# Kernel optimization log

Measured on AMD Instinct MI355X. Metric: run time of the kernel, lower is better.

## Reference

```python
import jax, jax.numpy as jnp
import numpy as np

# Llama-7B FFN up-proj quantized with HQQ 4-bit, group_size=64, axis=0
OUT, IN, GS = 11008, 4096, 64
G = OUT * IN // GS  # 704512 groups


def setup_inputs() -> dict:
    key = jax.random.key(0)
    k1, k2, k3, k4, k5 = jax.random.split(key, 5)
    # packed 4-bit weights: two nibbles per byte, shape [GS//2, G]
    W_q = jax.random.randint(k1, (GS // 2, G), 0, 256, dtype=jnp.int32)
    # per-group scale (meta['scale'] = 1/scale from quantize) and zero
    scale = jax.random.uniform(k2, (1, G), jnp.float32, minval=1e-3, maxval=1e-2)
    zero = jax.random.uniform(k3, (1, G), jnp.float32, minval=0.0, maxval=15.0)
    # decode-style activations: 8 sequences, 1 token each
    x = jax.random.normal(k4, (8, 1, IN), dtype=jnp.float32)
    bias = jax.random.normal(k5, (OUT,), dtype=jnp.float32) * 0.01
    return {"W_q": W_q, "scale": scale, "zero": zero, "x": x, "bias": bias}


def reference(W_q, scale, zero, x, bias):
    # BitPack.unpack_4bit_u8: high nibble rows stacked on low nibble rows
    hi = (W_q >> 4) & 0xF
    lo = W_q & 0xF
    W_q_p = jnp.concatenate([hi, lo], axis=0).astype(x.dtype)  # [GS, G]
    # Quantizer.dequantize: (W_q_p - zero) * scale, reshape to weight shape
    W_r = ((W_q_p - zero) * scale).reshape(OUT, IN)  # [out, in]
    # torch.nn.functional.linear(x, W_r, bias)
    return jnp.einsum('bsi,oi->bso', x, W_r) + bias
```

## Files before the change

### kernel.cpp

```cpp
#include <hip/hip_runtime.h>
#include <stdint.h>


#define OUT_ 11008
#define IN_ 4096
#define G_ 704512
#define OC_ 172
#define KS 8
#define KC (IN_ / KS)
#define TILE 256
#define NT (KC / TILE)

__device__ __forceinline__ void async_cp16(const void* gsrc, void* ldst) {
    __builtin_amdgcn_global_load_lds(
        (const __attribute__((address_space(1))) void*)gsrc,
        (__attribute__((address_space(3))) void*)ldst, 16, 0, 0);
}

__global__ __launch_bounds__(256, 3)
void hqq_gemv(const int* __restrict__ Wq, const float* __restrict__ scale,
              const float* __restrict__ zero, const float* __restrict__ x,
              float* __restrict__ ws) {
    __shared__ float x_lds[8 * KC];
    __shared__ float s_lds[KC];
    __shared__ float z_lds[KC];
    __shared__ int   wq_lds[2][16 * TILE];

    const int lane = threadIdx.x;
    const int ty   = threadIdx.y;
    const int oc   = blockIdx.y;
    const int ks   = blockIdx.z;
    const int rqb  = blockIdx.x * 16;

    const int kbase = ks * KC;
    const long gb = (long)oc * IN_ + kbase;

#pragma unroll
    for (int j = 0; j < 4; ++j) {
        const int fl = j * 1024 + ty * 256;
        const int b  = fl >> 9;
        const int k  = fl & (KC - 1);
        async_cp16(x + b * IN_ + kbase + k + lane * 4, x_lds + fl);
    }
    {
        const float* src = (ty < 2 ? scale : zero) + gb + (ty & 1) * 256 + lane * 4;
        float*       dst = (ty < 2 ? s_lds : z_lds) + (ty & 1) * 256;
        async_cp16(src, dst);
    }
#pragma unroll
    for (int j = 0; j < 4; ++j) {
        const int row = j * 4 + ty;
        async_cp16(Wq + (long)(rqb + row) * G_ + gb + lane * 4,
                   &wq_lds[0][row * TILE]);
    }
    __syncthreads();

    float acc[8][8];
#pragma unroll
    for (int r = 0; r < 8; ++r)
#pragma unroll
        for (int b = 0; b < 8; ++b) acc[r][b] = 0.f;

    const int i0 = lane * 4;

    for (int t = 0; t < NT; ++t) {
        const int buf = t & 1;
        if (t + 1 < NT) {
#pragma unroll
            for (int j = 0; j < 4; ++j) {
                const int row = j * 4 + ty;
                async_cp16(Wq + (long)(rqb + row) * G_ + gb + (t + 1) * TILE + lane * 4,
                           &wq_lds[buf ^ 1][row * TILE]);
            }
        }

        const int toff = t * TILE;
        const float4 s4 = *(const float4*)(s_lds + toff + i0);
        const float4 z4 = *(const float4*)(z_lds + toff + i0);
        const float ss[4] = {s4.x, s4.y, s4.z, s4.w};
        const float zs[4] = {-z4.x * s4.x, -z4.y * s4.y, -z4.z * s4.z, -z4.w * s4.w};

        float4 xv[8];
#pragma unroll
        for (int b = 0; b < 8; ++b)
            xv[b] = *(const float4*)(x_lds + b * KC + toff + i0);

#pragma unroll
        for (int rr = 0; rr < 4; ++rr) {
            const int4 q4 = *(const int4*)&wq_lds[buf][(ty * 4 + rr) * TILE + i0];
            const int qs[4] = {q4.x, q4.y, q4.z, q4.w};
            float wh[4], wl[4];
#pragma unroll
            for (int j = 0; j < 4; ++j) {
                wh[j] = fmaf((float)((qs[j] >> 4) & 0xF), ss[j], zs[j]);
                wl[j] = fmaf((float)( qs[j]       & 0xF), ss[j], zs[j]);
            }
#pragma unroll
            for (int b = 0; b < 8; ++b) {
                const float4 xb = xv[b];
                float ah = acc[rr * 2 + 0][b];
                float al = acc[rr * 2 + 1][b];
                ah = fmaf(xb.x, wh[0], ah); al = fmaf(xb.x, wl[0], al);
                ah = fmaf(xb.y, wh[1], ah); al = fmaf(xb.y, wl[1], al);
                ah = fmaf(xb.z, wh[2], ah); al = fmaf(xb.z, wl[2], al);
                ah = fmaf(xb.w, wh[3], ah); al = fmaf(xb.w, wl[3], al);
                acc[rr * 2 + 0][b] = ah;
                acc[rr * 2 + 1][b] = al;
            }
        }

        if (t + 1 < NT) __syncthreads();
    }

#pragma unroll
    for (int r = 0; r < 8; ++r)
#pragma unroll
        for (int b = 0; b < 8; ++b) {
            float v = acc[r][b];
#pragma unroll
            for (int off = 32; off > 0; off >>= 1)
                v += __shfl_down(v, off, 64);
            acc[r][b] = v;
        }

    if (lane == 0) {
        float* __restrict__ wp = ws + (long)ks * 8 * OUT_;
#pragma unroll
        for (int rr = 0; rr < 4; ++rr) {
            const int rq = rqb + ty * 4 + rr;
            const int o_hi = rq * OC_ + oc;
            const int o_lo = (rq + 32) * OC_ + oc;
#pragma unroll
            for (int b = 0; b < 8; ++b) {
                wp[b * OUT_ + o_hi] = acc[rr * 2 + 0][b];
                wp[b * OUT_ + o_lo] = acc[rr * 2 + 1][b];
            }
        }
    }
}

__global__ void hqq_reduce(const float* __restrict__ ws,
                           const float* __restrict__ bias,
                           float* __restrict__ out) {
    const int t = blockIdx.x * 256 + threadIdx.x;
    if (t >= 8 * OUT_) return;
    const int o = t % OUT_;
    float v = bias[o];
#pragma unroll
    for (int k = 0; k < KS; ++k) v += ws[k * 8 * OUT_ + t];
    out[t] = v;
}

extern "C" void kernel_launch(void* const* d_in, const int* in_sizes, int n_in,
                              void* d_out, int out_size, void* d_ws, size_t ws_size,
                              hipStream_t stream) {
    const int*   Wq    = (const int*)d_in[0];
    const float* scale = (const float*)d_in[1];
    const float* zero  = (const float*)d_in[2];
    const float* x     = (const float*)d_in[3];
    const float* bias  = (const float*)d_in[4];
    float* out = (float*)d_out;
    float* ws  = (float*)d_ws;

    dim3 grid(2, OC_, KS);
    dim3 block(64, 4);
    hqq_gemv<<<grid, block, 0, stream>>>(Wq, scale, zero, x, ws);
    hqq_reduce<<<(8 * OUT_ + 255) / 256, 256, 0, stream>>>(ws, bias, out);
}
```

Before: 171.4 us.

## Reduce K-split to 2 and stream x/scale/zero tiles through double buffers

The K-split factor drops from 8 to 2, giving fewer blocks that each run longer K loops. Activations, scales and zeros are no longer preloaded in full; they are now staged per tile into double-buffered LDS alongside the weights. This shrinks LDS use per block, cuts the split-K partial-sum traffic and reduce work, and overlaps all operand loads with compute. In exchange the grid has fewer blocks (688 instead of 2752), which may reduce parallelism on a large GPU, and a barrier now runs on every iteration.

```diff
diff --git a/kernel.cpp b/kernel.cpp
--- a/kernel.cpp
+++ b/kernel.cpp
@@ -6,7 +6,7 @@
 #define IN_ 4096
 #define G_ 704512
 #define OC_ 172
-#define KS 8
+#define KS 2
 #define KC (IN_ / KS)
 #define TILE 256
 #define NT (KC / TILE)
@@ -21,10 +21,10 @@
 void hqq_gemv(const int* __restrict__ Wq, const float* __restrict__ scale,
               const float* __restrict__ zero, const float* __restrict__ x,
               float* __restrict__ ws) {
-    __shared__ float x_lds[8 * KC];
-    __shared__ float s_lds[KC];
-    __shared__ float z_lds[KC];
     __shared__ int   wq_lds[2][16 * TILE];
+    __shared__ float x_lds[2][8 * TILE];
+    __shared__ float s_lds[2][TILE];
+    __shared__ float z_lds[2][TILE];
 
     const int lane = threadIdx.x;
     const int ty   = threadIdx.y;
@@ -34,26 +34,24 @@
 
     const int kbase = ks * KC;
     const long gb = (long)oc * IN_ + kbase;
+    const int i0 = lane * 4;
 
+    auto stage = [&](int t, int buf) {
+        const int koff = t * TILE;
 #pragma unroll
-    for (int j = 0; j < 4; ++j) {
-        const int fl = j * 1024 + ty * 256;
-        const int b  = fl >> 9;
-        const int k  = fl & (KC - 1);
-        async_cp16(x + b * IN_ + kbase + k + lane * 4, x_lds + fl);
-    }
-    {
-        const float* src = (ty < 2 ? scale : zero) + gb + (ty & 1) * 256 + lane * 4;
-        float*       dst = (ty < 2 ? s_lds : z_lds) + (ty & 1) * 256;
-        async_cp16(src, dst);
-    }
+        for (int j = 0; j < 4; ++j) {
+            const int row = j * 4 + ty;
+            async_cp16(Wq + (long)(rqb + row) * G_ + gb + koff + i0,
+                       &wq_lds[buf][row * TILE]);
+        }
 #pragma unroll
-    for (int j = 0; j < 4; ++j) {
-        const int row = j * 4 + ty;
-        async_cp16(Wq + (long)(rqb + row) * G_ + gb + lane * 4,
-                   &wq_lds[0][row * TILE]);
-    }
-    __syncthreads();
+        for (int j = 0; j < 2; ++j) {
+            const int b = ty * 2 + j;
+            async_cp16(x + b * IN_ + kbase + koff + i0, &x_lds[buf][b * TILE]);
+        }
+        if (ty == 0) async_cp16(scale + gb + koff + i0, &s_lds[buf][0]);
+        if (ty == 1) async_cp16(zero + gb + koff + i0, &z_lds[buf][0]);
+    };
 
     float acc[8][8];
 #pragma unroll
@@ -61,29 +59,22 @@
 #pragma unroll
         for (int b = 0; b < 8; ++b) acc[r][b] = 0.f;
 
-    const int i0 = lane * 4;
+    stage(0, 0);
+    __syncthreads();
 
+    int buf = 0;
     for (int t = 0; t < NT; ++t) {
-        const int buf = t & 1;
-        if (t + 1 < NT) {
-#pragma unroll
-            for (int j = 0; j < 4; ++j) {
-                const int row = j * 4 + ty;
-                async_cp16(Wq + (long)(rqb + row) * G_ + gb + (t + 1) * TILE + lane * 4,
-                           &wq_lds[buf ^ 1][row * TILE]);
-            }
-        }
+        if (t + 1 < NT) stage(t + 1, buf ^ 1);
 
-        const int toff = t * TILE;
-        const float4 s4 = *(const float4*)(s_lds + toff + i0);
-        const float4 z4 = *(const float4*)(z_lds + toff + i0);
+        const float4 s4 = *(const float4*)(&s_lds[buf][i0]);
+        const float4 z4 = *(const float4*)(&z_lds[buf][i0]);
         const float ss[4] = {s4.x, s4.y, s4.z, s4.w};
         const float zs[4] = {-z4.x * s4.x, -z4.y * s4.y, -z4.z * s4.z, -z4.w * s4.w};
 
         float4 xv[8];
 #pragma unroll
         for (int b = 0; b < 8; ++b)
-            xv[b] = *(const float4*)(x_lds + b * KC + toff + i0);
+            xv[b] = *(const float4*)(&x_lds[buf][b * TILE + i0]);
 
 #pragma unroll
         for (int rr = 0; rr < 4; ++rr) {
@@ -109,7 +100,8 @@
             }
         }
 
-        if (t + 1 < NT) __syncthreads();
+        __syncthreads();
+        buf ^= 1;
     }
 
 #pragma unroll
```

After: 156.1 us. 8.9% less time.
